# Kernel optimization log

Measured on AMD Instinct MI355X. Metric: run time of the kernel, lower is better.

Reference implementation:

```python
import jax, jax.numpy as jnp
import numpy as np

B, C, H, W = 16, 512, 48, 48


def setup_inputs() -> dict:
    key = jax.random.key(0)
    k1, k2 = jax.random.split(key)
    rgb = jax.random.normal(k1, (B, C, H, W), dtype=jnp.float32)
    depth = jax.random.normal(k2, (B, C, H, W), dtype=jnp.float32)
    return {"rgb": rgb, "depth": depth}


def reference(rgb, depth):
    b, c, h, w = rgb.shape
    hw = h * w
    q = rgb.reshape(b, c, hw)              # [B, C, HW]
    k = depth.reshape(b, c, hw)            # [B, C, HW]
    # channel-affinity: energy[b, i, j] = <rgb_chan_i, depth_chan_j>
    energy = jnp.einsum('bcn,bdn->bcd', q, k)   # [B, C, C]
    cl_index = jnp.argmax(energy, axis=2)       # [B, C] best-matching depth channel per rgb channel
    # gather matched depth channels and fuse
    gathered = depth[jnp.arange(b)[:, None], cl_index]  # [B, C, H, W]
    return rgb + gathered
```

## Files before the change

### kernel.cpp

```cpp
#include <hip/hip_runtime.h>
#include <stdint.h>

#define BATCH 16
#define CH    512
#define HW    2304
#define BM    128
#define BN    128

typedef _Float16 half8  __attribute__((ext_vector_type(8)));
typedef float    f32x16 __attribute__((ext_vector_type(16)));

#define MFMA16 __builtin_amdgcn_mfma_f32_32x32x16_f16

#define DELTA 3.5f

#define ENERGY_ELEMS ((size_t)BATCH * CH * CH)

__device__ __forceinline__ uint32_t f32_sortable(float f) {
    uint32_t u = __float_as_uint(f);
    return (u & 0x80000000u) ? ~u : (u | 0x80000000u);
}


#define BKs   64
#define NKTs  (HW / BKs)
#define AHs_OFF 0
#define BHs_OFF 16384
#define BUFs_SZ 32768

#define LGKM_BARRIER() do { \
    asm volatile("s_waitcnt lgkmcnt(0)" ::: "memory"); \
    __builtin_amdgcn_s_barrier(); \
    __builtin_amdgcn_sched_barrier(0); \
} while (0)

__device__ __forceinline__ int swzs(int r, int s) {
    return r * 128 + ((s ^ ((r >> 1) & 7)) << 4);
}

__device__ __forceinline__ half8 cvt8h(const float4& v0, const float4& v1) {
    half8 h;
    h[0] = (_Float16)v0.x; h[1] = (_Float16)v0.y;
    h[2] = (_Float16)v0.z; h[3] = (_Float16)v0.w;
    h[4] = (_Float16)v1.x; h[5] = (_Float16)v1.y;
    h[6] = (_Float16)v1.z; h[7] = (_Float16)v1.w;
    return h;
}

__device__ __forceinline__ void load_tile_s(const float* aG, const float* bG, int k0,
                                            float4 (&av)[4], float4 (&bv)[4]) {
    av[0] = *(const float4*)(aG + k0 + 0);
    av[1] = *(const float4*)(aG + k0 + 4);
    av[2] = *(const float4*)(aG + k0 + 8);
    av[3] = *(const float4*)(aG + k0 + 12);
    bv[0] = *(const float4*)(bG + k0 + 0);
    bv[1] = *(const float4*)(bG + k0 + 4);
    bv[2] = *(const float4*)(bG + k0 + 8);
    bv[3] = *(const float4*)(bG + k0 + 12);
}

__device__ __forceinline__ void stage_tile_s(char* dst,
                                             const float4 (&av)[4], const float4 (&bv)[4],
                                             int row, int q) {
    *(half8*)(dst + AHs_OFF + swzs(row, 2 * q))     = cvt8h(av[0], av[1]);
    *(half8*)(dst + AHs_OFF + swzs(row, 2 * q + 1)) = cvt8h(av[2], av[3]);
    *(half8*)(dst + BHs_OFF + swzs(row, 2 * q))     = cvt8h(bv[0], bv[1]);
    *(half8*)(dst + BHs_OFF + swzs(row, 2 * q + 1)) = cvt8h(bv[2], bv[3]);
}

__device__ __forceinline__ void compute_tile_s(const char* buf, int rA0, int rB, int half,
                                               f32x16& acc0, f32x16& acc1) {
    __builtin_amdgcn_s_setprio(1);
    #pragma unroll
    for (int kc = 0; kc < 4; ++kc) {
        const int s0 = 2 * kc + half;
        half8 ah0 = *(const half8*)(buf + AHs_OFF + swzs(rA0,      s0));
        half8 ah1 = *(const half8*)(buf + AHs_OFF + swzs(rA0 + 32, s0));
        half8 bh  = *(const half8*)(buf + BHs_OFF + swzs(rB, s0));
        acc0 = MFMA16(ah0, bh, acc0, 0, 0, 0);
        acc1 = MFMA16(ah1, bh, acc1, 0, 0, 0);
    }
    __builtin_amdgcn_s_setprio(0);
}

__global__ __launch_bounds__(512, 1)
void screen_kernel(const float* __restrict__ q,
                   const float* __restrict__ kmat,
                   float* __restrict__ energy)
{
    const int bid = blockIdx.x;
    const int nid = (bid & 7) * 32 + (bid >> 3);
    const int d0  = (nid & 3) * BN;
    const int c0  = ((nid >> 2) & 3) * BM;
    const int b   = nid >> 4;

    const int tid  = threadIdx.x;
    const int lane = tid & 63;
    const int w    = tid >> 6;
    const int wm   = w >> 2;
    const int wn   = w & 3;

    __shared__ __align__(16) char sm[2 * BUFs_SZ];
    char* buf0 = sm;
    char* buf1 = sm + BUFs_SZ;

    const float* qb = q    + (size_t)b * CH * HW;
    const float* kb = kmat + (size_t)b * CH * HW;

    const int row = tid >> 2, sq = tid & 3;
    const float* aG = qb + (size_t)(c0 + row) * HW + sq * 16;
    const float* bG = kb + (size_t)(d0 + row) * HW + sq * 16;

    float4 av0[4], bv0[4], av1[4], bv1[4];

    load_tile_s(aG, bG, 0, av0, bv0);
    stage_tile_s(buf0, av0, bv0, row, sq);
    load_tile_s(aG, bG, BKs, av1, bv1);
    LGKM_BARRIER();

    f32x16 acc0 = {}, acc1 = {};
    const int rA0  = wm * 64 + (lane & 31);
    const int rB   = wn * 32 + (lane & 31);
    const int half = lane >> 5;

    for (int kt = 0; kt < NKTs; kt += 2) {
        if (kt + 2 < NKTs) load_tile_s(aG, bG, (kt + 2) * BKs, av0, bv0);
        stage_tile_s(buf1, av1, bv1, row, sq);
        compute_tile_s(buf0, rA0, rB, half, acc0, acc1);
        LGKM_BARRIER();
        if (kt + 3 < NKTs) load_tile_s(aG, bG, (kt + 3) * BKs, av1, bv1);
        if (kt + 2 < NKTs) stage_tile_s(buf0, av0, bv0, row, sq);
        compute_tile_s(buf1, rA0, rB, half, acc0, acc1);
        LGKM_BARRIER();
    }

    float* eb = energy + ((size_t)(b * CH + c0) * CH) + d0 + wn * 32 + (lane & 31);
    #pragma unroll
    for (int mi = 0; mi < 2; ++mi) {
        #pragma unroll
        for (int qr = 0; qr < 16; ++qr) {
            int rowl = wm * 64 + mi * 32 + (qr & 3) + 8 * (qr >> 2) + 4 * (lane >> 5);
            eb[(size_t)rowl * CH] = (mi == 0) ? acc0[qr] : acc1[qr];
        }
    }
}

__global__ __launch_bounds__(256)
void rescore_gather_kernel(const float* __restrict__ rgb,
                           const float* __restrict__ depth,
                           const float* __restrict__ energy,
                           float* __restrict__ out)
{
    const int row = blockIdx.x;
    const int b   = row >> 9;
    const int tid = threadIdx.x;

    __shared__ float sred[4];
    __shared__ float sM;
    __shared__ int   scnt;
    __shared__ int   slist[CH];
    __shared__ unsigned long long sbest;

    const float* erow = energy + (size_t)row * CH;
    float e0 = erow[tid], e1 = erow[tid + 256];

    float m = fmaxf(e0, e1);
    #pragma unroll
    for (int off = 1; off < 64; off <<= 1) m = fmaxf(m, __shfl_xor(m, off, 64));
    if ((tid & 63) == 0) sred[tid >> 6] = m;
    __syncthreads();
    if (tid == 0) {
        sM = fmaxf(fmaxf(sred[0], sred[1]), fmaxf(sred[2], sred[3]));
        scnt = 0; sbest = 0ull;
    }
    __syncthreads();
    const float thr = sM - DELTA;
    if (e0 >= thr) { int i = atomicAdd(&scnt, 1); slist[i] = tid; }
    if (e1 >= thr) { int i = atomicAdd(&scnt, 1); slist[i] = tid + 256; }
    __syncthreads();
    const int cnt = scnt;

    const float4* q4 = (const float4*)(rgb + (size_t)row * HW);
    for (int i = 0; i < cnt; ++i) {
        const int d = slist[i];
        const float4* k4 = (const float4*)(depth + ((size_t)(b * CH + d)) * HW);
        float s = 0.0f;
        for (int j = tid; j < HW / 4; j += 256) {
            float4 a = q4[j], bb = k4[j];
            s += a.x * bb.x + a.y * bb.y + a.z * bb.z + a.w * bb.w;
        }
        #pragma unroll
        for (int off = 1; off < 64; off <<= 1) s += __shfl_xor(s, off, 64);
        if ((tid & 63) == 0) sred[tid >> 6] = s;
        __syncthreads();
        if (tid == 0) {
            float tot = sred[0] + sred[1] + sred[2] + sred[3];
            unsigned long long p =
                ((unsigned long long)f32_sortable(tot) << 32) |
                (uint32_t)(~(uint32_t)d);
            if (p > sbest) sbest = p;
        }
        __syncthreads();
    }

    const int widx = (int)(~(uint32_t)(sbest & 0xFFFFFFFFull));
    const float4* w4 = (const float4*)(depth + ((size_t)(b * CH + widx)) * HW);
    float4* o4 = (float4*)(out + (size_t)row * HW);
    for (int j = tid; j < HW / 4; j += 256) {
        float4 a = q4[j], dd = w4[j];
        o4[j] = make_float4(a.x + dd.x, a.y + dd.y, a.z + dd.z, a.w + dd.w);
    }
}


#define BKf 32
#define NKTf (HW / BKf)
#define AHf_OFF 0
#define ALf_OFF 16384
#define BHf_OFF 32768
#define BLf_OFF 49152
#define BUFf_SZ 65536

__device__ __forceinline__ int swzf(int r, int cb) {
    return r * 64 + (cb ^ (((r >> 1) & 3) << 4));
}

__device__ __forceinline__ void cvt8f(const float4& v0, const float4& v1,
                                      half8& h, half8& l) {
    float vv[8] = {v0.x, v0.y, v0.z, v0.w, v1.x, v1.y, v1.z, v1.w};
    #pragma unroll
    for (int j = 0; j < 8; ++j) {
        _Float16 hh = (_Float16)vv[j];
        h[j] = hh;
        l[j] = (_Float16)(vv[j] - (float)hh);
    }
}

#define AH8_OFF 0
#define AL8_OFF 8192
#define BH8_OFF 16384
#define BL8_OFF 24576
#define BUF8_SZ 32768

__device__ __forceinline__ void load_tile_f(const float* aG, const float* bG, int k0,
                                            float4 (&av)[2], float4 (&bv)[2], int qq) {
    av[0] = *(const float4*)(aG + k0 + qq * 8 + 0);
    av[1] = *(const float4*)(aG + k0 + qq * 8 + 4);
    bv[0] = *(const float4*)(bG + k0 + qq * 8 + 0);
    bv[1] = *(const float4*)(bG + k0 + qq * 8 + 4);
}

__device__ __forceinline__ void stage_tile_f(char* dst,
                                             const float4 (&av)[2], const float4 (&bv)[2],
                                             int row, int qq) {
    half8 h, l;
    cvt8f(av[0], av[1], h, l);
    *(half8*)(dst + AH8_OFF + swzf(row, qq * 16)) = h;
    *(half8*)(dst + AL8_OFF + swzf(row, qq * 16)) = l;
    cvt8f(bv[0], bv[1], h, l);
    *(half8*)(dst + BH8_OFF + swzf(row, qq * 16)) = h;
    *(half8*)(dst + BL8_OFF + swzf(row, qq * 16)) = l;
}

__device__ __forceinline__ void compute_tile_f(const char* buf, int rA0, int rB, int hb,
                                               f32x16& acc0, f32x16& acc1) {
    #pragma unroll
    for (int kc = 0; kc < 2; ++kc) {
        const int cb = kc * 32 + hb;
        half8 ah0 = *(const half8*)(buf + AH8_OFF + swzf(rA0,      cb));
        half8 ah1 = *(const half8*)(buf + AH8_OFF + swzf(rA0 + 32, cb));
        half8 al0 = *(const half8*)(buf + AL8_OFF + swzf(rA0,      cb));
        half8 al1 = *(const half8*)(buf + AL8_OFF + swzf(rA0 + 32, cb));
        half8 bh  = *(const half8*)(buf + BH8_OFF + swzf(rB, cb));
        half8 bl  = *(const half8*)(buf + BL8_OFF + swzf(rB, cb));
        acc0 = MFMA16(ah0, bh, acc0, 0, 0, 0);
        acc1 = MFMA16(ah1, bh, acc1, 0, 0, 0);
        acc0 = MFMA16(ah0, bl, acc0, 0, 0, 0);
        acc1 = MFMA16(ah1, bl, acc1, 0, 0, 0);
        acc0 = MFMA16(al0, bh, acc0, 0, 0, 0);
        acc1 = MFMA16(al1, bh, acc1, 0, 0, 0);
    }
}

__global__ __launch_bounds__(512, 1)
void fb_energy_argmax_kernel(const float* __restrict__ q,
                             const float* __restrict__ kmat,
                             unsigned long long* __restrict__ best)
{
    const int bid = blockIdx.x;
    const int nid = (bid & 7) * 32 + (bid >> 3);
    const int d0  = (nid & 3) * BN;
    const int c0  = ((nid >> 2) & 3) * BM;
    const int b   = nid >> 4;

    const int tid  = threadIdx.x;
    const int lane = tid & 63;
    const int w    = tid >> 6;
    const int wm   = w >> 2;
    const int wn   = w & 3;

    __shared__ __align__(16) char sm[2 * BUF8_SZ];
    char* buf0 = sm;
    char* buf1 = sm + BUF8_SZ;

    const float* qb = q    + (size_t)b * CH * HW;
    const float* kb = kmat + (size_t)b * CH * HW;

    const int row = tid >> 2, sq = tid & 3;
    const float* aG = qb + (size_t)(c0 + row) * HW;
    const float* bG = kb + (size_t)(d0 + row) * HW;

    float4 av0[2], bv0[2], av1[2], bv1[2];

    load_tile_f(aG, bG, 0, av0, bv0, sq);
    stage_tile_f(buf0, av0, bv0, row, sq);
    load_tile_f(aG, bG, BKf, av1, bv1, sq);
    __syncthreads();

    f32x16 acc0 = {}, acc1 = {};
    const int rA0 = wm * 64 + (lane & 31);
    const int rB  = wn * 32 + (lane & 31);
    const int hb  = (lane >> 5) * 16;

    for (int kt = 0; kt < NKTf; kt += 2) {
        if (kt + 2 < NKTf) load_tile_f(aG, bG, (kt + 2) * BKf, av0, bv0, sq);
        compute_tile_f(buf0, rA0, rB, hb, acc0, acc1);
        stage_tile_f(buf1, av1, bv1, row, sq);
        __syncthreads();
        if (kt + 3 < NKTf) load_tile_f(aG, bG, (kt + 3) * BKf, av1, bv1, sq);
        compute_tile_f(buf1, rA0, rB, hb, acc0, acc1);
        if (kt + 2 < NKTf) stage_tile_f(buf0, av0, bv0, row, sq);
        __syncthreads();
    }

    const uint32_t didx = ~(uint32_t)(d0 + wn * 32 + (lane & 31));
    #pragma unroll
    for (int mi = 0; mi < 2; ++mi) {
        #pragma unroll
        for (int qr = 0; qr < 16; ++qr) {
            float v = (mi == 0) ? acc0[qr] : acc1[qr];
            int rowl = wm * 64 + mi * 32 + (qr & 3) + 8 * (qr >> 2) + 4 * (lane >> 5);
            unsigned long long p =
                ((unsigned long long)f32_sortable(v) << 32) | didx;
            #pragma unroll
            for (int off = 1; off < 32; off <<= 1) {
                unsigned long long o = __shfl_xor(p, off, 64);
                if (o > p) p = o;
            }
            if ((lane & 31) == 0)
                atomicMax(&best[(size_t)b * CH + c0 + rowl], p);
        }
    }
}

__global__ __launch_bounds__(256)
void fb_gather_add_kernel(const float* __restrict__ rgb,
                          const float* __restrict__ depth,
                          const unsigned long long* __restrict__ best,
                          float* __restrict__ out)
{
    const int row = blockIdx.x;
    const int b   = row >> 9;
    const uint32_t idx = ~(uint32_t)(best[row] & 0xFFFFFFFFull);
    const float4* src = (const float4*)(rgb   + (size_t)row * HW);
    const float4* dep = (const float4*)(depth + ((size_t)b * CH + idx) * HW);
    float4*       dst = (float4*)(out + (size_t)row * HW);
    for (int j = threadIdx.x; j < HW / 4; j += 256) {
        float4 a = src[j], d = dep[j];
        dst[j] = make_float4(a.x + d.x, a.y + d.y, a.z + d.z, a.w + d.w);
    }
}

extern "C" void kernel_launch(void* const* d_in, const int* in_sizes, int n_in,
                              void* d_out, int out_size, void* d_ws, size_t ws_size,
                              hipStream_t stream)
{
    const float* rgb   = (const float*)d_in[0];
    const float* depth = (const float*)d_in[1];
    float* out = (float*)d_out;

    if (ws_size >= ENERGY_ELEMS * sizeof(float)) {
        float* energy = (float*)d_ws;
        screen_kernel<<<256, 512, 0, stream>>>(rgb, depth, energy);
        rescore_gather_kernel<<<BATCH * CH, 256, 0, stream>>>(rgb, depth, energy, out);
    } else {
        unsigned long long* best = (unsigned long long*)d_ws;
        hipMemsetAsync(best, 0, (size_t)BATCH * CH * sizeof(unsigned long long), stream);
        fb_energy_argmax_kernel<<<256, 512, 0, stream>>>(rgb, depth, best);
        fb_gather_add_kernel<<<BATCH * CH, 256, 0, stream>>>(rgb, depth, best, out);
    }
}
```

Baseline: 104.4 us.

## Pre-convert inputs to fp16 and stream tiles via direct global-to-LDS loads

Adds a conversion pass that writes fp16 copies of rgb and depth into workspace. A new screening GEMM reads those copies with global_load_lds DMA straight into swizzled shared memory, removing the per-tile register conversion and LDS staging. This halves the bytes the GEMM reads, at the cost of an extra full read-and-write pass over both inputs and a larger workspace requirement. It only runs when the workspace is large enough; the older fallback path is deleted and the screen kernel becomes the fallback.

```diff
diff --git a/kernel.cpp b/kernel.cpp
--- a/kernel.cpp
+++ b/kernel.cpp
@@ -14,13 +14,220 @@
 
 #define DELTA 3.5f
 
+#define N_ELEM       ((size_t)BATCH * CH * HW)
 #define ENERGY_ELEMS ((size_t)BATCH * CH * CH)
+#define WS_FAST16    (ENERGY_ELEMS * 4 + 2 * N_ELEM * 2)
 
 __device__ __forceinline__ uint32_t f32_sortable(float f) {
     uint32_t u = __float_as_uint(f);
     return (u & 0x80000000u) ? ~u : (u | 0x80000000u);
 }
 
+__global__ __launch_bounds__(256)
+void cvt_f16_kernel(const float* __restrict__ rgb, const float* __restrict__ depth,
+                    _Float16* __restrict__ rgb16, _Float16* __restrict__ depth16)
+{
+    const size_t stride = (size_t)gridDim.x * 256;
+    for (size_t i = (size_t)blockIdx.x * 256 + threadIdx.x; i < N_ELEM / 8; i += stride) {
+        float4 a0 = ((const float4*)rgb)[2 * i], a1 = ((const float4*)rgb)[2 * i + 1];
+        half8 h;
+        h[0] = (_Float16)a0.x; h[1] = (_Float16)a0.y;
+        h[2] = (_Float16)a0.z; h[3] = (_Float16)a0.w;
+        h[4] = (_Float16)a1.x; h[5] = (_Float16)a1.y;
+        h[6] = (_Float16)a1.z; h[7] = (_Float16)a1.w;
+        ((half8*)rgb16)[i] = h;
+        float4 b0 = ((const float4*)depth)[2 * i], b1 = ((const float4*)depth)[2 * i + 1];
+        half8 g;
+        g[0] = (_Float16)b0.x; g[1] = (_Float16)b0.y;
+        g[2] = (_Float16)b0.z; g[3] = (_Float16)b0.w;
+        g[4] = (_Float16)b1.x; g[5] = (_Float16)b1.y;
+        g[6] = (_Float16)b1.z; g[7] = (_Float16)b1.w;
+        ((half8*)depth16)[i] = g;
+    }
+}
+
+
+#define BK16    64
+#define NKT16   (HW / BK16)
+#define A16_OFF 0
+#define B16_OFF 16384
+#define BUF16_SZ 32768
+
+__device__ __forceinline__ void dma16(const _Float16* g, char* l) {
+    __builtin_amdgcn_global_load_lds(
+        (const __attribute__((address_space(1))) void*)g,
+        (__attribute__((address_space(3))) void*)l, 16, 0, 0);
+}
+
+__device__ __forceinline__ half8 rd16(const char* base, int r, int s0) {
+    return *(const half8*)(base + r * 128 + ((s0 ^ ((r >> 1) & 7)) << 4));
+}
+
+__device__ __forceinline__ void compute16(const char* buf, int rA0, int rB, int hf,
+                                          f32x16& acc0, f32x16& acc1) {
+    __builtin_amdgcn_s_setprio(1);
+    #pragma unroll
+    for (int kc = 0; kc < 4; ++kc) {
+        const int s0 = 2 * kc + hf;
+        half8 a0 = rd16(buf + A16_OFF, rA0,      s0);
+        half8 a1 = rd16(buf + A16_OFF, rA0 + 32, s0);
+        half8 bb = rd16(buf + B16_OFF, rB,       s0);
+        acc0 = MFMA16(a0, bb, acc0, 0, 0, 0);
+        acc1 = MFMA16(a1, bb, acc1, 0, 0, 0);
+    }
+    __builtin_amdgcn_s_setprio(0);
+}
+
+__global__ __launch_bounds__(512, 1)
+void screen16_kernel(const _Float16* __restrict__ q16,
+                     const _Float16* __restrict__ k16,
+                     float* __restrict__ energy)
+{
+    const int bid = blockIdx.x;
+    const int nid = (bid & 7) * 32 + (bid >> 3);
+    const int d0  = (nid & 3) * BN;
+    const int c0  = ((nid >> 2) & 3) * BM;
+    const int b   = nid >> 4;
+
+    const int tid  = threadIdx.x;
+    const int lane = tid & 63;
+    const int w    = tid >> 6;
+    const int wm   = w >> 2;
+    const int wn   = w & 3;
+
+    __shared__ __align__(16) char sm[2 * BUF16_SZ];
+
+    const _Float16* qb = q16 + (size_t)b * CH * HW;
+    const _Float16* kb = k16 + (size_t)b * CH * HW;
+
+    const int lr = lane >> 3, ls = lane & 7;
+    const int off0 = lr * HW + ((ls ^ (     (lr >> 1))) << 3);
+    const int off1 = lr * HW + ((ls ^ (4 + (lr >> 1))) << 3);
+    const _Float16* gA0 = qb + (size_t)(c0 + 16 * w)     * HW + off0;
+    const _Float16* gA1 = qb + (size_t)(c0 + 16 * w + 8) * HW + off1;
+    const _Float16* gB0 = kb + (size_t)(d0 + 16 * w)     * HW + off0;
+    const _Float16* gB1 = kb + (size_t)(d0 + 16 * w + 8) * HW + off1;
+
+    char* ldsA0o = sm + A16_OFF + (16 * w)     * 128;
+    char* ldsA1o = sm + A16_OFF + (16 * w + 8) * 128;
+    char* ldsB0o = sm + B16_OFF + (16 * w)     * 128;
+    char* ldsB1o = sm + B16_OFF + (16 * w + 8) * 128;
+
+    #define DMA_TILE(bufsel, t) do {                    \
+        const int ko_ = (t) * BK16;                     \
+        const size_t bo_ = (size_t)(bufsel) * BUF16_SZ; \
+        dma16(gA0 + ko_, ldsA0o + bo_);                 \
+        dma16(gA1 + ko_, ldsA1o + bo_);                 \
+        dma16(gB0 + ko_, ldsB0o + bo_);                 \
+        dma16(gB1 + ko_, ldsB1o + bo_);                 \
+    } while (0)
+
+    DMA_TILE(0, 0);
+    DMA_TILE(1, 1);
+    asm volatile("s_waitcnt vmcnt(4)" ::: "memory");
+    __builtin_amdgcn_sched_barrier(0);
+    __builtin_amdgcn_s_barrier();
+
+    f32x16 acc0 = {}, acc1 = {};
+    const int rA0 = wm * 64 + (lane & 31);
+    const int rB  = wn * 32 + (lane & 31);
+    const int hf  = lane >> 5;
+
+    for (int t = 0; t < NKT16; ++t) {
+        const char* rdb = sm + (size_t)(t & 1) * BUF16_SZ;
+        compute16(rdb, rA0, rB, hf, acc0, acc1);
+        if (t == NKT16 - 1) break;
+        asm volatile("s_waitcnt lgkmcnt(0)" ::: "memory");
+        __builtin_amdgcn_s_barrier();
+        __builtin_amdgcn_sched_barrier(0);
+        if (t + 2 < NKT16) {
+            DMA_TILE(t & 1, t + 2);
+            asm volatile("s_waitcnt vmcnt(4)" ::: "memory");
+        } else {
+            asm volatile("s_waitcnt vmcnt(0)" ::: "memory");
+        }
+        __builtin_amdgcn_sched_barrier(0);
+        __builtin_amdgcn_s_barrier();
+    }
+    #undef DMA_TILE
+
+    float* eb = energy + ((size_t)(b * CH + c0) * CH) + d0 + wn * 32 + (lane & 31);
+    #pragma unroll
+    for (int mi = 0; mi < 2; ++mi) {
+        #pragma unroll
+        for (int qr = 0; qr < 16; ++qr) {
+            int rowl = wm * 64 + mi * 32 + (qr & 3) + 8 * (qr >> 2) + 4 * (lane >> 5);
+            eb[(size_t)rowl * CH] = (mi == 0) ? acc0[qr] : acc1[qr];
+        }
+    }
+}
+
+__global__ __launch_bounds__(256)
+void rescore_gather_kernel(const float* __restrict__ rgb,
+                           const float* __restrict__ depth,
+                           const float* __restrict__ energy,
+                           float* __restrict__ out)
+{
+    const int row = blockIdx.x;
+    const int b   = row >> 9;
+    const int tid = threadIdx.x;
+
+    __shared__ float sred[4];
+    __shared__ float sM;
+    __shared__ int   scnt;
+    __shared__ int   slist[CH];
+    __shared__ unsigned long long sbest;
+
+    const float* erow = energy + (size_t)row * CH;
+    float e0 = erow[tid], e1 = erow[tid + 256];
+
+    float m = fmaxf(e0, e1);
+    #pragma unroll
+    for (int off = 1; off < 64; off <<= 1) m = fmaxf(m, __shfl_xor(m, off, 64));
+    if ((tid & 63) == 0) sred[tid >> 6] = m;
+    __syncthreads();
+    if (tid == 0) {
+        sM = fmaxf(fmaxf(sred[0], sred[1]), fmaxf(sred[2], sred[3]));
+        scnt = 0; sbest = 0ull;
+    }
+    __syncthreads();
+    const float thr = sM - DELTA;
+    if (e0 >= thr) { int i = atomicAdd(&scnt, 1); slist[i] = tid; }
+    if (e1 >= thr) { int i = atomicAdd(&scnt, 1); slist[i] = tid + 256; }
+    __syncthreads();
+    const int cnt = scnt;
+
+    const float4* q4 = (const float4*)(rgb + (size_t)row * HW);
+    for (int i = 0; i < cnt; ++i) {
+        const int d = slist[i];
+        const float4* k4 = (const float4*)(depth + ((size_t)(b * CH + d)) * HW);
+        float s = 0.0f;
+        for (int j = tid; j < HW / 4; j += 256) {
+            float4 a = q4[j], bb = k4[j];
+            s += a.x * bb.x + a.y * bb.y + a.z * bb.z + a.w * bb.w;
+        }
+        #pragma unroll
+        for (int off = 1; off < 64; off <<= 1) s += __shfl_xor(s, off, 64);
+        if ((tid & 63) == 0) sred[tid >> 6] = s;
+        __syncthreads();
+        if (tid == 0) {
+            float tot = sred[0] + sred[1] + sred[2] + sred[3];
+            unsigned long long p =
+                ((unsigned long long)f32_sortable(tot) << 32) |
+                (uint32_t)(~(uint32_t)d);
+            if (p > sbest) sbest = p;
+        }
+        __syncthreads();
+    }
+
+    const int widx = (int)(~(uint32_t)(sbest & 0xFFFFFFFFull));
+    const float4* w4 = (const float4*)(depth + ((size_t)(b * CH + widx)) * HW);
+    float4* o4 = (float4*)(out + (size_t)row * HW);
+    for (int j = tid; j < HW / 4; j += 256) {
+        float4 a = q4[j], dd = w4[j];
+        o4[j] = make_float4(a.x + dd.x, a.y + dd.y, a.z + dd.z, a.w + dd.w);
+    }
+}
 
 #define BKs   64
 #define NKTs  (HW / BKs)
@@ -145,232 +352,6 @@
     }
 }
 
-__global__ __launch_bounds__(256)
-void rescore_gather_kernel(const float* __restrict__ rgb,
-                           const float* __restrict__ depth,
-                           const float* __restrict__ energy,
-                           float* __restrict__ out)
-{
-    const int row = blockIdx.x;
-    const int b   = row >> 9;
-    const int tid = threadIdx.x;
-
-    __shared__ float sred[4];
-    __shared__ float sM;
-    __shared__ int   scnt;
-    __shared__ int   slist[CH];
-    __shared__ unsigned long long sbest;
-
-    const float* erow = energy + (size_t)row * CH;
-    float e0 = erow[tid], e1 = erow[tid + 256];
-
-    float m = fmaxf(e0, e1);
-    #pragma unroll
-    for (int off = 1; off < 64; off <<= 1) m = fmaxf(m, __shfl_xor(m, off, 64));
-    if ((tid & 63) == 0) sred[tid >> 6] = m;
-    __syncthreads();
-    if (tid == 0) {
-        sM = fmaxf(fmaxf(sred[0], sred[1]), fmaxf(sred[2], sred[3]));
-        scnt = 0; sbest = 0ull;
-    }
-    __syncthreads();
-    const float thr = sM - DELTA;
-    if (e0 >= thr) { int i = atomicAdd(&scnt, 1); slist[i] = tid; }
-    if (e1 >= thr) { int i = atomicAdd(&scnt, 1); slist[i] = tid + 256; }
-    __syncthreads();
-    const int cnt = scnt;
-
-    const float4* q4 = (const float4*)(rgb + (size_t)row * HW);
-    for (int i = 0; i < cnt; ++i) {
-        const int d = slist[i];
-        const float4* k4 = (const float4*)(depth + ((size_t)(b * CH + d)) * HW);
-        float s = 0.0f;
-        for (int j = tid; j < HW / 4; j += 256) {
-            float4 a = q4[j], bb = k4[j];
-            s += a.x * bb.x + a.y * bb.y + a.z * bb.z + a.w * bb.w;
-        }
-        #pragma unroll
-        for (int off = 1; off < 64; off <<= 1) s += __shfl_xor(s, off, 64);
-        if ((tid & 63) == 0) sred[tid >> 6] = s;
-        __syncthreads();
-        if (tid == 0) {
-            float tot = sred[0] + sred[1] + sred[2] + sred[3];
-            unsigned long long p =
-                ((unsigned long long)f32_sortable(tot) << 32) |
-                (uint32_t)(~(uint32_t)d);
-            if (p > sbest) sbest = p;
-        }
-        __syncthreads();
-    }
-
-    const int widx = (int)(~(uint32_t)(sbest & 0xFFFFFFFFull));
-    const float4* w4 = (const float4*)(depth + ((size_t)(b * CH + widx)) * HW);
-    float4* o4 = (float4*)(out + (size_t)row * HW);
-    for (int j = tid; j < HW / 4; j += 256) {
-        float4 a = q4[j], dd = w4[j];
-        o4[j] = make_float4(a.x + dd.x, a.y + dd.y, a.z + dd.z, a.w + dd.w);
-    }
-}
-
-
-#define BKf 32
-#define NKTf (HW / BKf)
-#define AHf_OFF 0
-#define ALf_OFF 16384
-#define BHf_OFF 32768
-#define BLf_OFF 49152
-#define BUFf_SZ 65536
-
-__device__ __forceinline__ int swzf(int r, int cb) {
-    return r * 64 + (cb ^ (((r >> 1) & 3) << 4));
-}
-
-__device__ __forceinline__ void cvt8f(const float4& v0, const float4& v1,
-                                      half8& h, half8& l) {
-    float vv[8] = {v0.x, v0.y, v0.z, v0.w, v1.x, v1.y, v1.z, v1.w};
-    #pragma unroll
-    for (int j = 0; j < 8; ++j) {
-        _Float16 hh = (_Float16)vv[j];
-        h[j] = hh;
-        l[j] = (_Float16)(vv[j] - (float)hh);
-    }
-}
-
-#define AH8_OFF 0
-#define AL8_OFF 8192
-#define BH8_OFF 16384
-#define BL8_OFF 24576
-#define BUF8_SZ 32768
-
-__device__ __forceinline__ void load_tile_f(const float* aG, const float* bG, int k0,
-                                            float4 (&av)[2], float4 (&bv)[2], int qq) {
-    av[0] = *(const float4*)(aG + k0 + qq * 8 + 0);
-    av[1] = *(const float4*)(aG + k0 + qq * 8 + 4);
-    bv[0] = *(const float4*)(bG + k0 + qq * 8 + 0);
-    bv[1] = *(const float4*)(bG + k0 + qq * 8 + 4);
-}
-
-__device__ __forceinline__ void stage_tile_f(char* dst,
-                                             const float4 (&av)[2], const float4 (&bv)[2],
-                                             int row, int qq) {
-    half8 h, l;
-    cvt8f(av[0], av[1], h, l);
-    *(half8*)(dst + AH8_OFF + swzf(row, qq * 16)) = h;
-    *(half8*)(dst + AL8_OFF + swzf(row, qq * 16)) = l;
-    cvt8f(bv[0], bv[1], h, l);
-    *(half8*)(dst + BH8_OFF + swzf(row, qq * 16)) = h;
-    *(half8*)(dst + BL8_OFF + swzf(row, qq * 16)) = l;
-}
-
-__device__ __forceinline__ void compute_tile_f(const char* buf, int rA0, int rB, int hb,
-                                               f32x16& acc0, f32x16& acc1) {
-    #pragma unroll
-    for (int kc = 0; kc < 2; ++kc) {
-        const int cb = kc * 32 + hb;
-        half8 ah0 = *(const half8*)(buf + AH8_OFF + swzf(rA0,      cb));
-        half8 ah1 = *(const half8*)(buf + AH8_OFF + swzf(rA0 + 32, cb));
-        half8 al0 = *(const half8*)(buf + AL8_OFF + swzf(rA0,      cb));
-        half8 al1 = *(const half8*)(buf + AL8_OFF + swzf(rA0 + 32, cb));
-        half8 bh  = *(const half8*)(buf + BH8_OFF + swzf(rB, cb));
-        half8 bl  = *(const half8*)(buf + BL8_OFF + swzf(rB, cb));
-        acc0 = MFMA16(ah0, bh, acc0, 0, 0, 0);
-        acc1 = MFMA16(ah1, bh, acc1, 0, 0, 0);
-        acc0 = MFMA16(ah0, bl, acc0, 0, 0, 0);
-        acc1 = MFMA16(ah1, bl, acc1, 0, 0, 0);
-        acc0 = MFMA16(al0, bh, acc0, 0, 0, 0);
-        acc1 = MFMA16(al1, bh, acc1, 0, 0, 0);
-    }
-}
-
-__global__ __launch_bounds__(512, 1)
-void fb_energy_argmax_kernel(const float* __restrict__ q,
-                             const float* __restrict__ kmat,
-                             unsigned long long* __restrict__ best)
-{
-    const int bid = blockIdx.x;
-    const int nid = (bid & 7) * 32 + (bid >> 3);
-    const int d0  = (nid & 3) * BN;
-    const int c0  = ((nid >> 2) & 3) * BM;
-    const int b   = nid >> 4;
-
-    const int tid  = threadIdx.x;
-    const int lane = tid & 63;
-    const int w    = tid >> 6;
-    const int wm   = w >> 2;
-    const int wn   = w & 3;
-
-    __shared__ __align__(16) char sm[2 * BUF8_SZ];
-    char* buf0 = sm;
-    char* buf1 = sm + BUF8_SZ;
-
-    const float* qb = q    + (size_t)b * CH * HW;
-    const float* kb = kmat + (size_t)b * CH * HW;
-
-    const int row = tid >> 2, sq = tid & 3;
-    const float* aG = qb + (size_t)(c0 + row) * HW;
-    const float* bG = kb + (size_t)(d0 + row) * HW;
-
-    float4 av0[2], bv0[2], av1[2], bv1[2];
-
-    load_tile_f(aG, bG, 0, av0, bv0, sq);
-    stage_tile_f(buf0, av0, bv0, row, sq);
-    load_tile_f(aG, bG, BKf, av1, bv1, sq);
-    __syncthreads();
-
-    f32x16 acc0 = {}, acc1 = {};
-    const int rA0 = wm * 64 + (lane & 31);
-    const int rB  = wn * 32 + (lane & 31);
-    const int hb  = (lane >> 5) * 16;
-
-    for (int kt = 0; kt < NKTf; kt += 2) {
-        if (kt + 2 < NKTf) load_tile_f(aG, bG, (kt + 2) * BKf, av0, bv0, sq);
-        compute_tile_f(buf0, rA0, rB, hb, acc0, acc1);
-        stage_tile_f(buf1, av1, bv1, row, sq);
-        __syncthreads();
-        if (kt + 3 < NKTf) load_tile_f(aG, bG, (kt + 3) * BKf, av1, bv1, sq);
-        compute_tile_f(buf1, rA0, rB, hb, acc0, acc1);
-        if (kt + 2 < NKTf) stage_tile_f(buf0, av0, bv0, row, sq);
-        __syncthreads();
-    }
-
-    const uint32_t didx = ~(uint32_t)(d0 + wn * 32 + (lane & 31));
-    #pragma unroll
-    for (int mi = 0; mi < 2; ++mi) {
-        #pragma unroll
-        for (int qr = 0; qr < 16; ++qr) {
-            float v = (mi == 0) ? acc0[qr] : acc1[qr];
-            int rowl = wm * 64 + mi * 32 + (qr & 3) + 8 * (qr >> 2) + 4 * (lane >> 5);
-            unsigned long long p =
-                ((unsigned long long)f32_sortable(v) << 32) | didx;
-            #pragma unroll
-            for (int off = 1; off < 32; off <<= 1) {
-                unsigned long long o = __shfl_xor(p, off, 64);
-                if (o > p) p = o;
-            }
-            if ((lane & 31) == 0)
-                atomicMax(&best[(size_t)b * CH + c0 + rowl], p);
-        }
-    }
-}
-
-__global__ __launch_bounds__(256)
-void fb_gather_add_kernel(const float* __restrict__ rgb,
-                          const float* __restrict__ depth,
-                          const unsigned long long* __restrict__ best,
-                          float* __restrict__ out)
-{
-    const int row = blockIdx.x;
-    const int b   = row >> 9;
-    const uint32_t idx = ~(uint32_t)(best[row] & 0xFFFFFFFFull);
-    const float4* src = (const float4*)(rgb   + (size_t)row * HW);
-    const float4* dep = (const float4*)(depth + ((size_t)b * CH + idx) * HW);
-    float4*       dst = (float4*)(out + (size_t)row * HW);
-    for (int j = threadIdx.x; j < HW / 4; j += 256) {
-        float4 a = src[j], d = dep[j];
-        dst[j] = make_float4(a.x + d.x, a.y + d.y, a.z + d.z, a.w + d.w);
-    }
-}
-
 extern "C" void kernel_launch(void* const* d_in, const int* in_sizes, int n_in,
                               void* d_out, int out_size, void* d_ws, size_t ws_size,
                               hipStream_t stream)
@@ -378,15 +359,16 @@
     const float* rgb   = (const float*)d_in[0];
     const float* depth = (const float*)d_in[1];
     float* out = (float*)d_out;
-
-    if (ws_size >= ENERGY_ELEMS * sizeof(float)) {
-        float* energy = (float*)d_ws;
+    float* energy = (float*)d_ws;
+
+    if (ws_size >= WS_FAST16) {
+        _Float16* rgb16   = (_Float16*)((char*)d_ws + ENERGY_ELEMS * 4);
+        _Float16* depth16 = rgb16 + N_ELEM;
+        cvt_f16_kernel<<<2048, 256, 0, stream>>>(rgb, depth, rgb16, depth16);
+        screen16_kernel<<<256, 512, 0, stream>>>(rgb16, depth16, energy);
+        rescore_gather_kernel<<<BATCH * CH, 256, 0, stream>>>(rgb, depth, energy, out);
+    } else {
         screen_kernel<<<256, 512, 0, stream>>>(rgb, depth, energy);
         rescore_gather_kernel<<<BATCH * CH, 256, 0, stream>>>(rgb, depth, energy, out);
-    } else {
-        unsigned long long* best = (unsigned long long*)d_ws;
-        hipMemsetAsync(best, 0, (size_t)BATCH * CH * sizeof(unsigned long long), stream);
-        fb_energy_argmax_kernel<<<256, 512, 0, stream>>>(rgb, depth, best);
-        fb_gather_add_kernel<<<BATCH * CH, 256, 0, stream>>>(rgb, depth, best, out);
-    }
-}
+    }
+}
```

Result: slower. 123.1 us (+18.0%).
